# Optimization experiments

Measured on AMD Instinct MI355X. Metric: run time of the kernel, lower is better.

The kernel has to match this reference:

```python
import jax, jax.numpy as jnp
import numpy as np


def setup_inputs() -> dict:
    key = jax.random.key(0)
    k1, k2, k3 = jax.random.split(key, 3)
    B, L, I = 128, 512, 1024
    doc_rep = jax.random.normal(k1, (B, L, I), dtype=jnp.float32)
    # torch.nn.Linear(input_size, label_size): weight (L, I), bias (L,)
    W = jax.random.normal(k2, (L, I), dtype=jnp.float32) * (1.0 / np.sqrt(I))
    b = jax.random.normal(k3, (L,), dtype=jnp.float32) * 0.01
    return {"doc_rep": doc_rep, "W": W, "b": b}


def reference(doc_rep, W, b):
    # Original: full Linear -> (B, L, L), then take diagonal over last two dims.
    # Diagonal of (doc_rep @ W.T + b) is exactly the per-label dot product:
    # out[b, l] = doc_rep[b, l, :] . W[l, :] + b[l]
    logits = jnp.einsum('bli,li->bl', doc_rep, W) + b
    return jax.nn.sigmoid(logits)
```

## Files before the change

### kernel.cpp

```cpp
#include <hip/hip_runtime.h>
#include <hip/hip_bf16.h>


#define B_DIM 128
#define L_DIM 512
#define I_DIM 1024

__global__ __launch_bounds__(256) void labelwise_mlc_kernel(
    const float* __restrict__ doc,
    const float* __restrict__ W,
    const float* __restrict__ bias,
    float* __restrict__ out)
{
    const int wave = (blockIdx.x * blockDim.x + threadIdx.x) >> 6;
    const int lane = threadIdx.x & 63;
    const int l = wave & (L_DIM - 1);

    const float4* __restrict__ dp =
        (const float4*)(doc + (size_t)wave * I_DIM);
    const float4* __restrict__ wp =
        (const float4*)(W + (size_t)l * I_DIM);

    float acc = 0.0f;
#pragma unroll
    for (int k = 0; k < 4; ++k) {
        const float4 d = dp[lane + 64 * k];
        const float4 w = wp[lane + 64 * k];
        acc = fmaf(d.x, w.x, acc);
        acc = fmaf(d.y, w.y, acc);
        acc = fmaf(d.z, w.z, acc);
        acc = fmaf(d.w, w.w, acc);
    }

#pragma unroll
    for (int off = 32; off > 0; off >>= 1)
        acc += __shfl_down(acc, off, 64);

    if (lane == 0) {
        const float v = acc + bias[l];
        out[wave] = 1.0f / (1.0f + __expf(-v));
    }
}

extern "C" void kernel_launch(void* const* d_in, const int* in_sizes, int n_in,
                              void* d_out, int out_size, void* d_ws, size_t ws_size,
                              hipStream_t stream) {
    const float* doc  = (const float*)d_in[0];
    const float* W    = (const float*)d_in[1];
    const float* bias = (const float*)d_in[2];
    float* out = (float*)d_out;

    const int n_out = B_DIM * L_DIM;
    const int blocks = n_out / 4;
    labelwise_mlc_kernel<<<blocks, 256, 0, stream>>>(doc, W, bias, out);
}
```

Measured before the change: 351.3 us.

## Reuse W row in registers across multiple batch rows per wave

Each wave now processes eight batch rows for a single label, loading the W row into registers once and reusing it. Doc loads become nontemporal to avoid polluting the cache. This cuts redundant W traffic and per-wave setup. The cost is 8x fewer waves and serialised iterations, which may reduce memory-level parallelism.

Measured after the change: 333.0 us (median of 2 runs). 5.2% less time.

```diff
diff --git a/kernel.cpp b/kernel.cpp
--- a/kernel.cpp
+++ b/kernel.cpp
@@ -5,6 +5,9 @@
 #define B_DIM 128
 #define L_DIM 512
 #define I_DIM 1024
+#define WPB 8
+
+typedef float vfloat4 __attribute__((ext_vector_type(4)));
 
 __global__ __launch_bounds__(256) void labelwise_mlc_kernel(
     const float* __restrict__ doc,
@@ -12,33 +15,38 @@
     const float* __restrict__ bias,
     float* __restrict__ out)
 {
-    const int wave = (blockIdx.x * blockDim.x + threadIdx.x) >> 6;
+    const int wave = (blockIdx.x * 256 + threadIdx.x) >> 6;
     const int lane = threadIdx.x & 63;
-    const int l = wave & (L_DIM - 1);
+    const int l  = wave & (L_DIM - 1);
+    const int b0 = (wave >> 9) * WPB;
 
-    const float4* __restrict__ dp =
-        (const float4*)(doc + (size_t)wave * I_DIM);
-    const float4* __restrict__ wp =
-        (const float4*)(W + (size_t)l * I_DIM);
+    const vfloat4* __restrict__ wp = (const vfloat4*)(W + (size_t)l * I_DIM);
+    vfloat4 w[4];
+#pragma unroll
+    for (int k = 0; k < 4; ++k) w[k] = wp[lane + 64 * k];
+    const float bl = bias[l];
 
-    float acc = 0.0f;
+#pragma unroll 2
+    for (int j = 0; j < WPB; ++j) {
+        const int b = b0 + j;
+        const vfloat4* __restrict__ dp =
+            (const vfloat4*)(doc + ((size_t)b * L_DIM + l) * I_DIM);
+        float acc = 0.0f;
 #pragma unroll
-    for (int k = 0; k < 4; ++k) {
-        const float4 d = dp[lane + 64 * k];
-        const float4 w = wp[lane + 64 * k];
-        acc = fmaf(d.x, w.x, acc);
-        acc = fmaf(d.y, w.y, acc);
-        acc = fmaf(d.z, w.z, acc);
-        acc = fmaf(d.w, w.w, acc);
-    }
-
+        for (int k = 0; k < 4; ++k) {
+            const vfloat4 d = __builtin_nontemporal_load(dp + lane + 64 * k);
+            acc = fmaf(d.x, w[k].x, acc);
+            acc = fmaf(d.y, w[k].y, acc);
+            acc = fmaf(d.z, w[k].z, acc);
+            acc = fmaf(d.w, w[k].w, acc);
+        }
 #pragma unroll
-    for (int off = 32; off > 0; off >>= 1)
-        acc += __shfl_down(acc, off, 64);
-
-    if (lane == 0) {
-        const float v = acc + bias[l];
-        out[wave] = 1.0f / (1.0f + __expf(-v));
+        for (int off = 32; off > 0; off >>= 1)
+            acc += __shfl_down(acc, off, 64);
+        if (lane == 0) {
+            const float v = acc + bl;
+            out[(size_t)b * L_DIM + l] = 1.0f / (1.0f + __expf(-v));
+        }
     }
 }
 
@@ -50,7 +58,6 @@
     const float* bias = (const float*)d_in[2];
     float* out = (float*)d_out;
 
-    const int n_out = B_DIM * L_DIM;
-    const int blocks = n_out / 4;
+    const int blocks = (L_DIM * (B_DIM / WPB)) / 4;
     labelwise_mlc_kernel<<<blocks, 256, 0, stream>>>(doc, W, bias, out);
 }
```
